# Kernel optimization log

Hardware: AMD Instinct MI355X
Metric: run time of the kernel (lower is better)

Reference implementation:

```python
import jax, jax.numpy as jnp
import numpy as np

N, E, B = 10000, 100000, 64
VOCAB, EMB, H = 5000, 100, 2000
LAYERS = 4


def setup_inputs() -> dict:
    key = jax.random.key(0)
    ks = jax.random.split(key, 12)
    s = 0.02
    tokens = jax.random.randint(ks[0], (N,), 0, VOCAB)
    edge_index = jax.random.randint(ks[1], (2, E), 0, N)
    batch = (jnp.arange(N) * B) // N  # sorted node->graph ids, every graph nonempty
    return {
        "tokens": tokens,
        "edge_index": edge_index,
        "batch": batch,
        "embed_table": jax.random.normal(ks[2], (VOCAB, EMB), jnp.float32) * s,
        "W_ggc": jax.random.normal(ks[3], (LAYERS, H, H), jnp.float32) * s,
        "W_ih": jax.random.normal(ks[4], (3 * H, H), jnp.float32) * s,
        "W_hh": jax.random.normal(ks[5], (3 * H, H), jnp.float32) * s,
        "b_ih": jnp.zeros((3 * H,), jnp.float32),
        "b_hh": jnp.zeros((3 * H,), jnp.float32),
        "conv1_w": jax.random.normal(ks[6], (50, 1, 3), jnp.float32) * s,
        "conv1_b": jnp.zeros((50,), jnp.float32),
        "conv2_w": jax.random.normal(ks[7], (100, 50, 3), jnp.float32) * s,
        "conv2_b": jnp.zeros((100,), jnp.float32),
        "conv3_w": jax.random.normal(ks[8], (150, 100, 3), jnp.float32) * s,
        "conv3_b": jnp.zeros((150,), jnp.float32),
        "lin1_w": jax.random.normal(ks[9], (500, 10950), jnp.float32) * s,
        "lin1_b": jnp.zeros((500,), jnp.float32),
        "lin2_w": jax.random.normal(ks[10], (4, 500), jnp.float32) * s,
        "lin2_b": jnp.zeros((4,), jnp.float32),
    }


def _conv1d(x, w, b):
    # x: [B, Cin, L], w: [Cout, Cin, K] -> [B, Cout, L-K+1] (VALID, like nn.Conv1d)
    y = jax.lax.conv_general_dilated(x, w, (1,), "VALID",
                                     dimension_numbers=("NCH", "OIH", "NCH"))
    return y + b[None, :, None]


def _maxpool3(x):
    # MaxPool1d(kernel=3, stride=3), floor mode (VALID)
    return jax.lax.reduce_window(x, -jnp.inf, jax.lax.max, (1, 1, 3), (1, 1, 3), "VALID")


def _gru_cell(m, h, W_ih, W_hh, b_ih, b_hh):
    gi = m @ W_ih.T + b_ih  # [N, 3H]
    gh = h @ W_hh.T + b_hh
    ir, iz, inn = jnp.split(gi, 3, axis=-1)
    hr, hz, hn = jnp.split(gh, 3, axis=-1)
    r = jax.nn.sigmoid(ir + hr)
    z = jax.nn.sigmoid(iz + hz)
    n = jnp.tanh(inn + r * hn)
    return (1.0 - z) * n + z * h


def reference(tokens, edge_index, batch, embed_table, W_ggc, W_ih, W_hh, b_ih, b_hh,
              conv1_w, conv1_b, conv2_w, conv2_b, conv3_w, conv3_b,
              lin1_w, lin1_b, lin2_w, lin2_b):
    src, dst = edge_index[0], edge_index[1]
    n_nodes = tokens.shape[0]
    # embedding + pad to GatedGraphConv width (PyG zero-pads when in < out)
    h = embed_table[tokens]                               # [N, 100]
    h = jnp.pad(h, ((0, 0), (0, H - h.shape[1])))         # [N, 2000]
    # GatedGraphConv: per-layer linear -> scatter-add over edges -> GRU update
    for i in range(LAYERS):
        m = h @ W_ggc[i]                                  # [N, H]
        agg = jax.ops.segment_sum(m[src], dst, num_segments=n_nodes)  # [N, H]
        h = _gru_cell(agg, h, W_ih, W_hh, b_ih, b_hh)
    x = jax.nn.relu(h)
    # global_max_pool over graphs
    pooled = jax.ops.segment_max(x, batch, num_segments=B)  # [B, 2000]
    x = pooled[:, None, :]                                  # [B, 1, 2000]
    x = _maxpool3(jax.nn.relu(_conv1d(x, conv1_w, conv1_b)))  # [B,50,666]
    x = _maxpool3(jax.nn.relu(_conv1d(x, conv2_w, conv2_b)))  # [B,100,221]
    x = _maxpool3(jax.nn.relu(_conv1d(x, conv3_w, conv3_b)))  # [B,150,73]
    x = x.reshape(x.shape[0], -1)                             # [B, 10950]
    x = jax.nn.relu(x @ lin1_w.T + lin1_b)
    # dropout is identity in eval mode
    x = jax.nn.relu(x @ lin2_w.T + lin2_b)
    return x
```

## Files before the change

kernel.cpp:

```cpp
#include <hip/hip_runtime.h>
#include <math.h>

#define N_NODES 10000
#define N_EDGES 100000
#define NB      64
#define EMB     100
#define H       2000
#define LAYERS  4

#define C1_OC 50
#define C1_L  666
#define C2_OC 100
#define C2_L  221
#define C3_OC 150
#define C3_L  73
#define LIN1_IN  10950
#define LIN1_OUT 500

#define SEG  2048
#define MP   10240
#define NW   2048
#define KK2  4096
#define NPACK 8192
#define NT   (KK2 / 64)

using half8 = __attribute__((ext_vector_type(8))) _Float16;
using f32x4 = __attribute__((ext_vector_type(4))) float;

__device__ inline void gload16(const void* g, void* l) {
  __builtin_amdgcn_global_load_lds(
      (const __attribute__((address_space(1))) unsigned int*)g,
      (__attribute__((address_space(3))) unsigned int*)l, 16, 0, 0);
}

__global__ void embed16_kernel(const int* __restrict__ tokens,
                               const float* __restrict__ table,
                               _Float16* __restrict__ h) {
  int n = blockIdx.x;
  int tok = tokens[n];
  for (int c = threadIdx.x; c < SEG; c += 256) {
    float v = (c < EMB) ? table[tok * EMB + c] : 0.f;
    h[(size_t)n * SEG + c] = (_Float16)v;
  }
}

__global__ void hist_kernel(const int* __restrict__ dst, int* __restrict__ counts, int e) {
  int i = blockIdx.x * 256 + threadIdx.x;
  if (i < e) atomicAdd(&counts[dst[i]], 1);
}

__global__ void scan_kernel(const int* __restrict__ counts, int* __restrict__ row_off, int n) {
  __shared__ int sums[1024];
  int tid = threadIdx.x;
  const int CH = (n + 1023) / 1024;
  int start = tid * CH;
  int local = 0;
  for (int i = 0; i < CH; i++)
    if (start + i < n) local += counts[start + i];
  sums[tid] = local;
  __syncthreads();
  for (int off = 1; off < 1024; off <<= 1) {
    int v = (tid >= off) ? sums[tid - off] : 0;
    __syncthreads();
    sums[tid] += v;
    __syncthreads();
  }
  int run = (tid > 0) ? sums[tid - 1] : 0;
  for (int i = 0; i < CH; i++)
    if (start + i < n) { row_off[start + i] = run; run += counts[start + i]; }
  if (tid == 1023) row_off[n] = run;
}

__global__ void scatter_kernel(const int* __restrict__ src, const int* __restrict__ dst,
                               const int* __restrict__ row_off, int* __restrict__ cursor,
                               int* __restrict__ csr_src, int e) {
  int i = blockIdx.x * 256 + threadIdx.x;
  if (i < e) {
    int d = dst[i];
    int pos = atomicAdd(&cursor[d], 1);
    csr_src[row_off[d] + pos] = src[i];
  }
}

__global__ void starts_kernel(const int* __restrict__ batch, int* __restrict__ starts, int n) {
  int i = blockIdx.x * 256 + threadIdx.x;
  if (i >= n) return;
  int b = batch[i];
  int pb = (i == 0) ? -1 : batch[i - 1];
  if (b != pb)
    for (int x = pb + 1; x <= b; x++) starts[x] = i;
  if (i == n - 1)
    for (int x = b + 1; x <= NB; x++) starts[x] = n;
}

__global__ void prep_wg16_kernel(const float* __restrict__ Wg, _Float16* __restrict__ out) {
  __shared__ float t[32][33];
  int l = blockIdx.z;
  const float* W = Wg + (size_t)l * H * H;
  _Float16* o = out + (size_t)l * NW * SEG;
  int kt = blockIdx.x * 32, nt = blockIdx.y * 32;
  int tx = threadIdx.x & 31, ty = threadIdx.x >> 5;
#pragma unroll
  for (int i = 0; i < 4; i++) {
    int k = kt + ty + i * 8, n = nt + tx;
    t[tx][ty + i * 8] = (k < H && n < H) ? W[(size_t)k * H + n] : 0.f;
  }
  __syncthreads();
#pragma unroll
  for (int i = 0; i < 4; i++) {
    int nl = ty + i * 8, kl = tx;
    o[(size_t)(nt + nl) * SEG + (kt + kl)] = (_Float16)t[nl][kl];
  }
}

__global__ void prep_wpack_kernel(const float* __restrict__ Wih, const float* __restrict__ Whh,
                                  _Float16* __restrict__ out) {
  int n = blockIdx.y;
  int k = blockIdx.x * 256 + threadIdx.x;
  if (k >= KK2) return;
  int gate = ((n >> 7) & 1) * 2 + ((n >> 4) & 1);
  int hcol = (n >> 8) * 64 + ((n >> 5) & 3) * 16 + (n & 15);
  float v = 0.f;
  if (hcol < H) {
    if (gate < 2) {
      int row = gate * H + hcol;
      if (k < 2048) { if (k < H) v = Wih[(size_t)row * H + k]; }
      else { int k2 = k - 2048; if (k2 < H) v = Whh[(size_t)row * H + k2]; }
    } else if (gate == 2) {
      if (k < H) v = Wih[(size_t)(2 * H + hcol) * H + k];
    } else {
      int k2 = k - 2048;
      if (k2 >= 0 && k2 < H) v = Whh[(size_t)(2 * H + hcol) * H + k2];
    }
  }
  out[(size_t)n * KK2 + k] = (_Float16)v;
}

__global__ __launch_bounds__(256) void gemm16_kernel(
    const _Float16* __restrict__ A, const _Float16* __restrict__ Bt,
    _Float16* __restrict__ C) {
  __shared__ __align__(16) _Float16 As[128][32];
  __shared__ __align__(16) _Float16 Bs[128][32];
  const int tid = threadIdx.x;
  const int wave = tid >> 6, lane = tid & 63;
  const int bm = blockIdx.y * 128, bn = blockIdx.x * 128;
  const int wm = (wave & 1) * 64, wn = (wave >> 1) * 64;
  const int srow = lane >> 2, scol = (lane & 3) * 8;
  const int fr = lane & 15, quad = lane >> 4;

  f32x4 acc[4][4];
#pragma unroll
  for (int i = 0; i < 4; i++)
#pragma unroll
    for (int j = 0; j < 4; j++) {
      f32x4 z = {0.f, 0.f, 0.f, 0.f};
      acc[i][j] = z;
    }

  for (int k0 = 0; k0 < SEG; k0 += 32) {
    gload16(A + (size_t)(bm + wave * 32 + srow) * SEG + k0 + scol, &As[wave * 32][0]);
    gload16(A + (size_t)(bm + wave * 32 + 16 + srow) * SEG + k0 + scol, &As[wave * 32 + 16][0]);
    gload16(Bt + (size_t)(bn + wave * 32 + srow) * SEG + k0 + scol, &Bs[wave * 32][0]);
    gload16(Bt + (size_t)(bn + wave * 32 + 16 + srow) * SEG + k0 + scol, &Bs[wave * 32 + 16][0]);
    __syncthreads();
    half8 af[4], bf[4];
#pragma unroll
    for (int i = 0; i < 4; i++) {
      af[i] = *(const half8*)&As[wm + i * 16 + fr][quad * 8];
      bf[i] = *(const half8*)&Bs[wn + i * 16 + fr][quad * 8];
    }
#pragma unroll
    for (int i = 0; i < 4; i++)
#pragma unroll
      for (int j = 0; j < 4; j++)
        acc[i][j] = __builtin_amdgcn_mfma_f32_16x16x32_f16(af[i], bf[j], acc[i][j], 0, 0, 0);
    __syncthreads();
  }
#pragma unroll
  for (int i = 0; i < 4; i++)
#pragma unroll
    for (int j = 0; j < 4; j++) {
      int n = bn + wn + j * 16 + fr;
      if (n >= SEG) continue;
#pragma unroll
      for (int r = 0; r < 4; r++) {
        int m = bm + wm + i * 16 + quad * 4 + r;
        C[(size_t)m * SEG + n] = (_Float16)acc[i][j][r];
      }
    }
}

__global__ void agg16_kernel(const _Float16* __restrict__ m, const int* __restrict__ row_off,
                             const int* __restrict__ csr_src, _Float16* __restrict__ agg) {
  int node = blockIdx.x;
  int s = row_off[node], e = row_off[node + 1];
  int tid = threadIdx.x;
  bool act = tid < (SEG / 8);
  float a[8] = {0, 0, 0, 0, 0, 0, 0, 0};
  __shared__ int s_src[256];
  for (int base = s; base < e; base += 256) {
    int cnt = min(256, e - base);
    __syncthreads();
    if (tid < cnt) s_src[tid] = csr_src[base + tid];
    __syncthreads();
    for (int p = 0; p < cnt; p++) {
      if (act) {
        half8 v = *(const half8*)&m[(size_t)s_src[p] * SEG + tid * 8];
#pragma unroll
        for (int i = 0; i < 8; i++) a[i] += (float)v[i];
      }
    }
  }
  if (act) {
    half8 o;
#pragma unroll
    for (int i = 0; i < 8; i++) o[i] = (_Float16)a[i];
    *(half8*)&agg[(size_t)node * SEG + tid * 8] = o;
  }
}

__global__ __launch_bounds__(512, 2) void gru2p_kernel(
    const _Float16* __restrict__ Agg, const _Float16* __restrict__ Hc,
    const _Float16* __restrict__ Wp,
    const float* __restrict__ b_ih, const float* __restrict__ b_hh,
    _Float16* __restrict__ Hn) {
  __shared__ __align__(16) _Float16 As[2][256][64];
  __shared__ __align__(16) _Float16 Bs[2][256][64];
  const int tid = threadIdx.x;
  const int wave = tid >> 6, lane = tid & 63;
  const int WM = wave >> 2, WN = wave & 3;
  const int fr = lane & 15, quad = lane >> 4;
  const int bm = blockIdx.y * 256, bn = blockIdx.x * 256;

  const int sr = lane >> 3;
  const int scl = (lane & 7) ^ sr;

  auto stageA = [&](int buf, int hf, int t) {
    const _Float16* base = (t < 32) ? Agg : Hc;
    const int k0 = (t & 31) * 64;
    const int r0 = hf * 128 + wave * 8 + sr;
#pragma unroll
    for (int c2 = 0; c2 < 2; c2++) {
      gload16(base + (size_t)(bm + r0 + c2 * 64) * SEG + k0 + scl * 8,
              &As[buf][hf * 128 + c2 * 64 + wave * 8][0]);
    }
  };
  auto stageB = [&](int buf, int hf, int t) {
    const int k0 = t * 64;
    const int r0 = hf * 128 + wave * 8 + sr;
#pragma unroll
    for (int c2 = 0; c2 < 2; c2++) {
      gload16(Wp + (size_t)(bn + r0 + c2 * 64) * KK2 + k0 + scl * 8,
              &Bs[buf][hf * 128 + c2 * 64 + wave * 8][0]);
    }
  };

  const int x0 = ((quad ^ (fr & 7)) << 3);
  const int x1 = (((quad + 4) ^ (fr & 7)) << 3);

  auto readA = [&](int buf, int mh, half8* a) {
    const _Float16* base = &As[buf][mh * 128 + WM * 64][0];
#pragma unroll
    for (int i = 0; i < 4; i++) {
      const int rb = ((i << 4) + fr) << 6;
      a[i]     = *(const half8*)&base[rb + x0];
      a[4 + i] = *(const half8*)&base[rb + x1];
    }
  };
  auto readB = [&](int buf, int nh, int j, half8* b) {
    const _Float16* base = &Bs[buf][nh * 128 + WN * 32 + (j << 4) + fr][0];
    b[0] = *(const half8*)&base[x0];
    b[1] = *(const half8*)&base[x1];
  };

  f32x4 acc[2][4][4];
#pragma unroll
  for (int a = 0; a < 2; a++)
#pragma unroll
    for (int i = 0; i < 4; i++)
#pragma unroll
      for (int g = 0; g < 4; g++) {
        f32x4 z = {0.f, 0.f, 0.f, 0.f};
        acc[a][i][g] = z;
      }

  stageA(0, 0, 0); stageA(0, 1, 0); stageB(0, 0, 0); stageB(0, 1, 0);
  stageA(1, 0, 1); stageB(1, 0, 1);
  asm volatile("s_waitcnt vmcnt(4)" ::: "memory");
  __builtin_amdgcn_s_barrier();

  half8 a0[8], a1[8], b0[2], b1[2], bx[2], bxn[2];
  readA(0, 0, a0);
  readB(0, 0, 0, b0);
  readB(0, 0, 1, b1);
  readB(0, 1, 0, bx);

  for (int t = 0; t < NT; t++) {
    const int cur = t & 1, nxt = cur ^ 1;
    const bool firstHalf = (t < 32);

    if (t + 1 < NT) { stageA(nxt, 1, t + 1); stageB(nxt, 1, t + 1); }
    asm volatile("s_waitcnt lgkmcnt(0)" ::: "memory");
    __builtin_amdgcn_sched_barrier(0);
    __builtin_amdgcn_s_barrier();
    readA(cur, 1, a1);
    __builtin_amdgcn_sched_barrier(0);
    __builtin_amdgcn_s_setprio(1);
#pragma unroll
    for (int i = 0; i < 4; i++) {
      acc[0][i][0] = __builtin_amdgcn_mfma_f32_16x16x32_f16(a0[i], b0[0], acc[0][i][0], 0, 0, 0);
      acc[0][i][1] = __builtin_amdgcn_mfma_f32_16x16x32_f16(a0[i], b1[0], acc[0][i][1], 0, 0, 0);
      acc[0][i][0] = __builtin_amdgcn_mfma_f32_16x16x32_f16(a0[4 + i], b0[1], acc[0][i][0], 0, 0, 0);
      acc[0][i][1] = __builtin_amdgcn_mfma_f32_16x16x32_f16(a0[4 + i], b1[1], acc[0][i][1], 0, 0, 0);
    }
    if (firstHalf) {
#pragma unroll
      for (int i = 0; i < 4; i++) {
        acc[0][i][2] = __builtin_amdgcn_mfma_f32_16x16x32_f16(a0[i], bx[0], acc[0][i][2], 0, 0, 0);
        acc[0][i][2] = __builtin_amdgcn_mfma_f32_16x16x32_f16(a0[4 + i], bx[1], acc[0][i][2], 0, 0, 0);
      }
    } else {
#pragma unroll
      for (int i = 0; i < 4; i++) {
        acc[0][i][3] = __builtin_amdgcn_mfma_f32_16x16x32_f16(a0[i], bx[0], acc[0][i][3], 0, 0, 0);
        acc[0][i][3] = __builtin_amdgcn_mfma_f32_16x16x32_f16(a0[4 + i], bx[1], acc[0][i][3], 0, 0, 0);
      }
    }
    __builtin_amdgcn_s_setprio(0);

    if (t + 2 < NT) {
      stageA(cur, 0, t + 2); stageB(cur, 0, t + 2);
      asm volatile("s_waitcnt vmcnt(4)" ::: "memory");
    } else {
      asm volatile("s_waitcnt vmcnt(0)" ::: "memory");
    }
    asm volatile("s_waitcnt lgkmcnt(0)" ::: "memory");
    __builtin_amdgcn_sched_barrier(0);
    __builtin_amdgcn_s_barrier();
    __builtin_amdgcn_s_setprio(1);
#pragma unroll
    for (int i = 0; i < 4; i++) {
      acc[1][i][0] = __builtin_amdgcn_mfma_f32_16x16x32_f16(a1[i], b0[0], acc[1][i][0], 0, 0, 0);
      acc[1][i][1] = __builtin_amdgcn_mfma_f32_16x16x32_f16(a1[i], b1[0], acc[1][i][1], 0, 0, 0);
      acc[1][i][0] = __builtin_amdgcn_mfma_f32_16x16x32_f16(a1[4 + i], b0[1], acc[1][i][0], 0, 0, 0);
      acc[1][i][1] = __builtin_amdgcn_mfma_f32_16x16x32_f16(a1[4 + i], b1[1], acc[1][i][1], 0, 0, 0);
    }
    __builtin_amdgcn_s_setprio(0);
    __builtin_amdgcn_sched_barrier(0);
    if (t + 1 < NT) {
      readA(nxt, 0, a0);
      readB(nxt, 0, 0, b0);
      readB(nxt, 0, 1, b1);
      readB(nxt, 1, ((t + 1) < 32) ? 0 : 1, bxn);
    }
    __builtin_amdgcn_sched_barrier(0);
    __builtin_amdgcn_s_setprio(1);
    if (firstHalf) {
#pragma unroll
      for (int i = 0; i < 4; i++) {
        acc[1][i][2] = __builtin_amdgcn_mfma_f32_16x16x32_f16(a1[i], bx[0], acc[1][i][2], 0, 0, 0);
        acc[1][i][2] = __builtin_amdgcn_mfma_f32_16x16x32_f16(a1[4 + i], bx[1], acc[1][i][2], 0, 0, 0);
      }
    } else {
#pragma unroll
      for (int i = 0; i < 4; i++) {
        acc[1][i][3] = __builtin_amdgcn_mfma_f32_16x16x32_f16(a1[i], bx[0], acc[1][i][3], 0, 0, 0);
        acc[1][i][3] = __builtin_amdgcn_mfma_f32_16x16x32_f16(a1[4 + i], bx[1], acc[1][i][3], 0, 0, 0);
      }
    }
    __builtin_amdgcn_s_setprio(0);
    bx[0] = bxn[0]; bx[1] = bxn[1];
  }

  const int c = blockIdx.x * 64 + WN * 16 + fr;
  if (c >= H) return;
  const float b_r = b_ih[c] + b_hh[c];
  const float b_z = b_ih[H + c] + b_hh[H + c];
  const float b_in = b_ih[2 * H + c];
  const float b_hn = b_hh[2 * H + c];
#pragma unroll
  for (int mh = 0; mh < 2; mh++)
#pragma unroll
    for (int i = 0; i < 4; i++)
#pragma unroll
      for (int r = 0; r < 4; r++) {
        int m = bm + mh * 128 + WM * 64 + i * 16 + quad * 4 + r;
        float rg = 1.f / (1.f + expf(-(acc[mh][i][0][r] + b_r)));
        float zg = 1.f / (1.f + expf(-(acc[mh][i][1][r] + b_z)));
        float nn = tanhf(acc[mh][i][2][r] + b_in + rg * (acc[mh][i][3][r] + b_hn));
        float hold = (float)Hc[(size_t)m * SEG + c];
        Hn[(size_t)m * SEG + c] = (_Float16)((1.f - zg) * nn + zg * hold);
      }
}

__global__ void pool16_kernel(const _Float16* __restrict__ h, const int* __restrict__ starts,
                              float* __restrict__ pooled) {
  int b = blockIdx.x;
  int s = starts[b], e = starts[b + 1];
  for (int idx = threadIdx.x; idx < H; idx += 256) {
    float mx = 0.f;
    for (int n = s; n < e; n++) mx = fmaxf(mx, (float)h[(size_t)n * SEG + idx]);
    pooled[b * H + idx] = mx;
  }
}

__global__ void conv1_kernel(const float* __restrict__ in, const float* __restrict__ w,
                             const float* __restrict__ bias, float* __restrict__ outp) {
  __shared__ float sin_[H];
  int b = blockIdx.x;
  for (int j = threadIdx.x; j < H; j += 256) sin_[j] = in[(size_t)b * H + j];
  __syncthreads();
  for (int idx = threadIdx.x; idx < C1_OC * C1_L; idx += 256) {
    int oc = idx / C1_L, t = idx % C1_L;
    float w0 = w[oc * 3], w1 = w[oc * 3 + 1], w2 = w[oc * 3 + 2];
    float bb = bias[oc];
    float best = 0.f;
    int base = t * 3;
#pragma unroll
    for (int p = 0; p < 3; p++) {
      float v = fmaf(sin_[base + p], w0, fmaf(sin_[base + p + 1], w1,
                fmaf(sin_[base + p + 2], w2, bb)));
      best = fmaxf(best, v);
    }
    outp[((size_t)b * C1_OC + oc) * C1_L + t] = best;
  }
}

__global__ void conv2_kernel(const float* __restrict__ in, const float* __restrict__ w,
                             const float* __restrict__ bias, float* __restrict__ outp) {
  int idx = blockIdx.x * 256 + threadIdx.x;
  if (idx >= NB * C2_OC * C2_L) return;
  int t = idx % C2_L;
  int rem = idx / C2_L;
  int oc = rem % C2_OC;
  int b = rem / C2_OC;
  const float* ip = in + (size_t)b * C1_OC * C1_L;
  const float* wp = w + oc * C1_OC * 3;
  float bb = bias[oc];
  float s0 = bb, s1 = bb, s2 = bb;
  int tc = t * 3;
  for (int ic = 0; ic < C1_OC; ic++) {
    const float* r = ip + ic * C1_L + tc;
    float v0 = r[0], v1 = r[1], v2 = r[2], v3 = r[3], v4 = r[4];
    float w0 = wp[ic * 3], w1 = wp[ic * 3 + 1], w2 = wp[ic * 3 + 2];
    s0 = fmaf(v0, w0, fmaf(v1, w1, fmaf(v2, w2, s0)));
    s1 = fmaf(v1, w0, fmaf(v2, w1, fmaf(v3, w2, s1)));
    s2 = fmaf(v2, w0, fmaf(v3, w1, fmaf(v4, w2, s2)));
  }
  outp[idx] = fmaxf(fmaxf(s0, fmaxf(s1, s2)), 0.f);
}

__global__ void conv3_kernel(const float* __restrict__ in, const float* __restrict__ w,
                             const float* __restrict__ bias, float* __restrict__ outp) {
  int idx = blockIdx.x * 256 + threadIdx.x;
  if (idx >= NB * C3_OC * C3_L) return;
  int t = idx % C3_L;
  int rem = idx / C3_L;
  int oc = rem % C3_OC;
  int b = rem / C3_OC;
  const float* ip = in + (size_t)b * C2_OC * C2_L;
  const float* wp = w + oc * C2_OC * 3;
  float bb = bias[oc];
  float s0 = bb, s1 = bb, s2 = bb;
  int tc = t * 3;
  for (int ic = 0; ic < C2_OC; ic++) {
    const float* r = ip + ic * C2_L + tc;
    float v0 = r[0], v1 = r[1], v2 = r[2], v3 = r[3], v4 = r[4];
    float w0 = wp[ic * 3], w1 = wp[ic * 3 + 1], w2 = wp[ic * 3 + 2];
    s0 = fmaf(v0, w0, fmaf(v1, w1, fmaf(v2, w2, s0)));
    s1 = fmaf(v1, w0, fmaf(v2, w1, fmaf(v3, w2, s1)));
    s2 = fmaf(v2, w0, fmaf(v3, w1, fmaf(v4, w2, s2)));
  }
  outp[idx] = fmaxf(fmaxf(s0, fmaxf(s1, s2)), 0.f);
}

__global__ void lin1_kernel(const float* __restrict__ x, const float* __restrict__ w,
                            const float* __restrict__ bias, float* __restrict__ outp) {
  int gid = blockIdx.x * 4 + (threadIdx.x >> 6);
  int lane = threadIdx.x & 63;
  int b = gid / LIN1_OUT;
  int o = gid % LIN1_OUT;
  const float* xp = x + (size_t)b * LIN1_IN;
  const float* wp = w + (size_t)o * LIN1_IN;
  float s = 0.f;
  for (int k = lane; k < LIN1_IN; k += 64) s = fmaf(xp[k], wp[k], s);
#pragma unroll
  for (int off = 32; off > 0; off >>= 1) s += __shfl_down(s, off, 64);
  if (lane == 0) outp[b * LIN1_OUT + o] = fmaxf(s + bias[o], 0.f);
}

__global__ void lin2_kernel(const float* __restrict__ x, const float* __restrict__ w,
                            const float* __restrict__ bias, float* __restrict__ outp) {
  int tid = threadIdx.x;
  int b = tid >> 2, o = tid & 3;
  const float* xp = x + b * LIN1_OUT;
  const float* wp = w + o * LIN1_OUT;
  float s = bias[o];
  for (int k = 0; k < LIN1_OUT; k++) s = fmaf(xp[k], wp[k], s);
  outp[b * 4 + o] = fmaxf(s, 0.f);
}

extern "C" void kernel_launch(void* const* d_in, const int* in_sizes, int n_in,
                              void* d_out, int out_size, void* d_ws, size_t ws_size,
                              hipStream_t stream) {
  const int* tokens = (const int*)d_in[0];
  const int* edge_index = (const int*)d_in[1];
  const int* batch = (const int*)d_in[2];
  const float* embed = (const float*)d_in[3];
  const float* W_ggc = (const float*)d_in[4];
  const float* W_ih = (const float*)d_in[5];
  const float* W_hh = (const float*)d_in[6];
  const float* b_ih = (const float*)d_in[7];
  const float* b_hh = (const float*)d_in[8];
  const float* c1w = (const float*)d_in[9];
  const float* c1b = (const float*)d_in[10];
  const float* c2w = (const float*)d_in[11];
  const float* c2b = (const float*)d_in[12];
  const float* c3w = (const float*)d_in[13];
  const float* c3b = (const float*)d_in[14];
  const float* l1w = (const float*)d_in[15];
  const float* l1b = (const float*)d_in[16];
  const float* l2w = (const float*)d_in[17];
  const float* l2b = (const float*)d_in[18];
  float* out = (float*)d_out;

  const int* e_src = edge_index;
  const int* e_dst = edge_index + N_EDGES;

  char* ws = (char*)d_ws;
  size_t off = 0;
  auto alloc = [&](size_t bytes) -> void* {
    void* p = ws + off;
    off = (off + bytes + 255) & ~(size_t)255;
    return p;
  };

  const size_t ACT = sizeof(_Float16) * (size_t)MP * SEG;
  _Float16* bufX = (_Float16*)alloc(ACT);
  _Float16* bufY = (_Float16*)alloc(ACT);
  _Float16* bufZ = (_Float16*)alloc(ACT);
  _Float16* Wg_b = (_Float16*)alloc(sizeof(_Float16) * (size_t)LAYERS * NW * SEG);
  _Float16* Wp   = (_Float16*)alloc(sizeof(_Float16) * (size_t)NPACK * KK2);
  int* counts = (int*)alloc(sizeof(int) * (N_NODES + 1));
  int* row_off = (int*)alloc(sizeof(int) * (N_NODES + 1));
  int* cursor = (int*)alloc(sizeof(int) * N_NODES);
  int* csr_src = (int*)alloc(sizeof(int) * N_EDGES);
  int* starts = (int*)alloc(sizeof(int) * (NB + 1));

  char* tb = (char*)bufZ;
  size_t toff = 0;
  auto talloc = [&](size_t bytes) -> void* {
    void* p = tb + toff;
    toff = (toff + bytes + 255) & ~(size_t)255;
    return p;
  };
  float* pooled = (float*)talloc(sizeof(float) * NB * H);
  float* c1 = (float*)talloc(sizeof(float) * (size_t)NB * C1_OC * C1_L);
  float* c2 = (float*)talloc(sizeof(float) * (size_t)NB * C2_OC * C2_L);
  float* c3 = (float*)talloc(sizeof(float) * (size_t)NB * C3_OC * C3_L);
  float* l1out = (float*)talloc(sizeof(float) * NB * LIN1_OUT);

  hipMemsetAsync(counts, 0, sizeof(int) * (N_NODES + 1), stream);
  hipMemsetAsync(cursor, 0, sizeof(int) * N_NODES, stream);

  {
    dim3 gg(SEG / 32, NW / 32, LAYERS);
    prep_wg16_kernel<<<gg, 256, 0, stream>>>(W_ggc, Wg_b);
    dim3 gp(KK2 / 256, NPACK);
    prep_wpack_kernel<<<gp, 256, 0, stream>>>(W_ih, W_hh, Wp);
  }

  embed16_kernel<<<N_NODES, 256, 0, stream>>>(tokens, embed, bufX);
  hist_kernel<<<(N_EDGES + 255) / 256, 256, 0, stream>>>(e_dst, counts, N_EDGES);
  scan_kernel<<<1, 1024, 0, stream>>>(counts, row_off, N_NODES);
  scatter_kernel<<<(N_EDGES + 255) / 256, 256, 0, stream>>>(e_src, e_dst, row_off, cursor,
                                                            csr_src, N_EDGES);
  starts_kernel<<<(N_NODES + 255) / 256, 256, 0, stream>>>(batch, starts, N_NODES);

  dim3 grid_m(NW / 128, MP / 128);
  dim3 grid_gru(NPACK / 256, MP / 256);
  _Float16* X = bufX;
  _Float16* Y = bufY;
  for (int l = 0; l < LAYERS; l++) {
    gemm16_kernel<<<grid_m, 256, 0, stream>>>(X, Wg_b + (size_t)l * NW * SEG, Y);
    agg16_kernel<<<N_NODES, 256, 0, stream>>>(Y, row_off, csr_src, bufZ);
    gru2p_kernel<<<grid_gru, 512, 0, stream>>>(bufZ, X, Wp, b_ih, b_hh, Y);
    _Float16* t = X; X = Y; Y = t;
  }

  pool16_kernel<<<NB, 256, 0, stream>>>(X, starts, pooled);
  conv1_kernel<<<NB, 256, 0, stream>>>(pooled, c1w, c1b, c1);
  conv2_kernel<<<(NB * C2_OC * C2_L + 255) / 256, 256, 0, stream>>>(c1, c2w, c2b, c2);
  conv3_kernel<<<(NB * C3_OC * C3_L + 255) / 256, 256, 0, stream>>>(c2, c3w, c3b, c3);
  lin1_kernel<<<NB * LIN1_OUT / 4, 256, 0, stream>>>(c3, l1w, l1b, l1out);
  lin2_kernel<<<1, 256, 0, stream>>>(l1out, l2w, l2b, out);
}
```

Baseline: 4.744 ms.

## Restructure GRU GEMM main loop to one barrier-phase with in-iteration LDS reads

Reorganises the software pipeline of the fused GRU GEMM. Each iteration now reads the current A/B fragments from LDS at its top instead of prefetching the next tile's registers at its end. The next-half and next-tile global stages are issued earlier, and MFMAs are grouped per A half (both gates plus the n-gate block together). The aim is to cut register pressure, drop the cross-iteration register handoff and one barrier-separated phase, and interleave LDS reads with MFMA issue. The cost is that LDS latency is exposed at the start of each iteration, since it is no longer hidden behind the previous MFMAs.

Result: slower. 6.785 ms (+43.0%).

```diff
diff --git a/kernel.cpp b/kernel.cpp
--- a/kernel.cpp
+++ b/kernel.cpp
@@ -219,7 +219,7 @@
   }
 }
 
-__global__ __launch_bounds__(512, 2) void gru2p_kernel(
+__global__ __launch_bounds__(512, 2) void gruv3_kernel(
     const _Float16* __restrict__ Agg, const _Float16* __restrict__ Hc,
     const _Float16* __restrict__ Wp,
     const float* __restrict__ b_ih, const float* __restrict__ b_hh,
@@ -289,87 +289,80 @@
   asm volatile("s_waitcnt vmcnt(4)" ::: "memory");
   __builtin_amdgcn_s_barrier();
 
-  half8 a0[8], a1[8], b0[2], b1[2], bx[2], bxn[2];
-  readA(0, 0, a0);
-  readB(0, 0, 0, b0);
-  readB(0, 0, 1, b1);
-  readB(0, 1, 0, bx);
-
   for (int t = 0; t < NT; t++) {
     const int cur = t & 1, nxt = cur ^ 1;
     const bool firstHalf = (t < 32);
 
+    __builtin_amdgcn_sched_barrier(0);
+    half8 a0[8], a1[8], b0[2], b1[2], bx[2];
+    readA(cur, 0, a0);
+    readB(cur, 0, 0, b0);
+    readB(cur, 0, 1, b1);
+    readB(cur, 1, firstHalf ? 0 : 1, bx);
     if (t + 1 < NT) { stageA(nxt, 1, t + 1); stageB(nxt, 1, t + 1); }
     asm volatile("s_waitcnt lgkmcnt(0)" ::: "memory");
     __builtin_amdgcn_sched_barrier(0);
     __builtin_amdgcn_s_barrier();
+    __builtin_amdgcn_sched_barrier(0);
+
     readA(cur, 1, a1);
+    if (t + 2 < NT) { stageA(cur, 0, t + 2); stageB(cur, 0, t + 2); }
+    __builtin_amdgcn_s_setprio(1);
+    if (firstHalf) {
+#pragma unroll
+      for (int i = 0; i < 4; i++) {
+        acc[0][i][0] = __builtin_amdgcn_mfma_f32_16x16x32_f16(a0[i], b0[0], acc[0][i][0], 0, 0, 0);
+        acc[0][i][1] = __builtin_amdgcn_mfma_f32_16x16x32_f16(a0[i], b1[0], acc[0][i][1], 0, 0, 0);
+        acc[0][i][2] = __builtin_amdgcn_mfma_f32_16x16x32_f16(a0[i], bx[0], acc[0][i][2], 0, 0, 0);
+        acc[0][i][0] = __builtin_amdgcn_mfma_f32_16x16x32_f16(a0[4 + i], b0[1], acc[0][i][0], 0, 0, 0);
+        acc[0][i][1] = __builtin_amdgcn_mfma_f32_16x16x32_f16(a0[4 + i], b1[1], acc[0][i][1], 0, 0, 0);
+        acc[0][i][2] = __builtin_amdgcn_mfma_f32_16x16x32_f16(a0[4 + i], bx[1], acc[0][i][2], 0, 0, 0);
+      }
+    } else {
+#pragma unroll
+      for (int i = 0; i < 4; i++) {
+        acc[0][i][0] = __builtin_amdgcn_mfma_f32_16x16x32_f16(a0[i], b0[0], acc[0][i][0], 0, 0, 0);
+        acc[0][i][1] = __builtin_amdgcn_mfma_f32_16x16x32_f16(a0[i], b1[0], acc[0][i][1], 0, 0, 0);
+        acc[0][i][3] = __builtin_amdgcn_mfma_f32_16x16x32_f16(a0[i], bx[0], acc[0][i][3], 0, 0, 0);
+        acc[0][i][0] = __builtin_amdgcn_mfma_f32_16x16x32_f16(a0[4 + i], b0[1], acc[0][i][0], 0, 0, 0);
+        acc[0][i][1] = __builtin_amdgcn_mfma_f32_16x16x32_f16(a0[4 + i], b1[1], acc[0][i][1], 0, 0, 0);
+        acc[0][i][3] = __builtin_amdgcn_mfma_f32_16x16x32_f16(a0[4 + i], bx[1], acc[0][i][3], 0, 0, 0);
+      }
+    }
+    __builtin_amdgcn_s_setprio(0);
+    asm volatile("s_waitcnt lgkmcnt(0)" ::: "memory");
     __builtin_amdgcn_sched_barrier(0);
+
     __builtin_amdgcn_s_setprio(1);
-#pragma unroll
-    for (int i = 0; i < 4; i++) {
-      acc[0][i][0] = __builtin_amdgcn_mfma_f32_16x16x32_f16(a0[i], b0[0], acc[0][i][0], 0, 0, 0);
-      acc[0][i][1] = __builtin_amdgcn_mfma_f32_16x16x32_f16(a0[i], b1[0], acc[0][i][1], 0, 0, 0);
-      acc[0][i][0] = __builtin_amdgcn_mfma_f32_16x16x32_f16(a0[4 + i], b0[1], acc[0][i][0], 0, 0, 0);
-      acc[0][i][1] = __builtin_amdgcn_mfma_f32_16x16x32_f16(a0[4 + i], b1[1], acc[0][i][1], 0, 0, 0);
-    }
     if (firstHalf) {
 #pragma unroll
       for (int i = 0; i < 4; i++) {
-        acc[0][i][2] = __builtin_amdgcn_mfma_f32_16x16x32_f16(a0[i], bx[0], acc[0][i][2], 0, 0, 0);
-        acc[0][i][2] = __builtin_amdgcn_mfma_f32_16x16x32_f16(a0[4 + i], bx[1], acc[0][i][2], 0, 0, 0);
+        acc[1][i][0] = __builtin_amdgcn_mfma_f32_16x16x32_f16(a1[i], b0[0], acc[1][i][0], 0, 0, 0);
+        acc[1][i][1] = __builtin_amdgcn_mfma_f32_16x16x32_f16(a1[i], b1[0], acc[1][i][1], 0, 0, 0);
+        acc[1][i][2] = __builtin_amdgcn_mfma_f32_16x16x32_f16(a1[i], bx[0], acc[1][i][2], 0, 0, 0);
+        acc[1][i][0] = __builtin_amdgcn_mfma_f32_16x16x32_f16(a1[4 + i], b0[1], acc[1][i][0], 0, 0, 0);
+        acc[1][i][1] = __builtin_amdgcn_mfma_f32_16x16x32_f16(a1[4 + i], b1[1], acc[1][i][1], 0, 0, 0);
+        acc[1][i][2] = __builtin_amdgcn_mfma_f32_16x16x32_f16(a1[4 + i], bx[1], acc[1][i][2], 0, 0, 0);
       }
     } else {
 #pragma unroll
       for (int i = 0; i < 4; i++) {
-        acc[0][i][3] = __builtin_amdgcn_mfma_f32_16x16x32_f16(a0[i], bx[0], acc[0][i][3], 0, 0, 0);
-        acc[0][i][3] = __builtin_amdgcn_mfma_f32_16x16x32_f16(a0[4 + i], bx[1], acc[0][i][3], 0, 0, 0);
+        acc[1][i][0] = __builtin_amdgcn_mfma_f32_16x16x32_f16(a1[i], b0[0], acc[1][i][0], 0, 0, 0);
+        acc[1][i][1] = __builtin_amdgcn_mfma_f32_16x16x32_f16(a1[i], b1[0], acc[1][i][1], 0, 0, 0);
+        acc[1][i][3] = __builtin_amdgcn_mfma_f32_16x16x32_f16(a1[i], bx[0], acc[1][i][3], 0, 0, 0);
+        acc[1][i][0] = __builtin_amdgcn_mfma_f32_16x16x32_f16(a1[4 + i], b0[1], acc[1][i][0], 0, 0, 0);
+        acc[1][i][1] = __builtin_amdgcn_mfma_f32_16x16x32_f16(a1[4 + i], b1[1], acc[1][i][1], 0, 0, 0);
+        acc[1][i][3] = __builtin_amdgcn_mfma_f32_16x16x32_f16(a1[4 + i], bx[1], acc[1][i][3], 0, 0, 0);
       }
     }
     __builtin_amdgcn_s_setprio(0);
 
     if (t + 2 < NT) {
-      stageA(cur, 0, t + 2); stageB(cur, 0, t + 2);
       asm volatile("s_waitcnt vmcnt(4)" ::: "memory");
     } else {
       asm volatile("s_waitcnt vmcnt(0)" ::: "memory");
     }
-    asm volatile("s_waitcnt lgkmcnt(0)" ::: "memory");
-    __builtin_amdgcn_sched_barrier(0);
     __builtin_amdgcn_s_barrier();
-    __builtin_amdgcn_s_setprio(1);
-#pragma unroll
-    for (int i = 0; i < 4; i++) {
-      acc[1][i][0] = __builtin_amdgcn_mfma_f32_16x16x32_f16(a1[i], b0[0], acc[1][i][0], 0, 0, 0);
-      acc[1][i][1] = __builtin_amdgcn_mfma_f32_16x16x32_f16(a1[i], b1[0], acc[1][i][1], 0, 0, 0);
-      acc[1][i][0] = __builtin_amdgcn_mfma_f32_16x16x32_f16(a1[4 + i], b0[1], acc[1][i][0], 0, 0, 0);
-      acc[1][i][1] = __builtin_amdgcn_mfma_f32_16x16x32_f16(a1[4 + i], b1[1], acc[1][i][1], 0, 0, 0);
-    }
-    __builtin_amdgcn_s_setprio(0);
-    __builtin_amdgcn_sched_barrier(0);
-    if (t + 1 < NT) {
-      readA(nxt, 0, a0);
-      readB(nxt, 0, 0, b0);
-      readB(nxt, 0, 1, b1);
-      readB(nxt, 1, ((t + 1) < 32) ? 0 : 1, bxn);
-    }
-    __builtin_amdgcn_sched_barrier(0);
-    __builtin_amdgcn_s_setprio(1);
-    if (firstHalf) {
-#pragma unroll
-      for (int i = 0; i < 4; i++) {
-        acc[1][i][2] = __builtin_amdgcn_mfma_f32_16x16x32_f16(a1[i], bx[0], acc[1][i][2], 0, 0, 0);
-        acc[1][i][2] = __builtin_amdgcn_mfma_f32_16x16x32_f16(a1[4 + i], bx[1], acc[1][i][2], 0, 0, 0);
-      }
-    } else {
-#pragma unroll
-      for (int i = 0; i < 4; i++) {
-        acc[1][i][3] = __builtin_amdgcn_mfma_f32_16x16x32_f16(a1[i], bx[0], acc[1][i][3], 0, 0, 0);
-        acc[1][i][3] = __builtin_amdgcn_mfma_f32_16x16x32_f16(a1[4 + i], bx[1], acc[1][i][3], 0, 0, 0);
-      }
-    }
-    __builtin_amdgcn_s_setprio(0);
-    bx[0] = bxn[0]; bx[1] = bxn[1];
   }
 
   const int c = blockIdx.x * 64 + WN * 16 + fr;
@@ -584,7 +577,7 @@
   for (int l = 0; l < LAYERS; l++) {
     gemm16_kernel<<<grid_m, 256, 0, stream>>>(X, Wg_b + (size_t)l * NW * SEG, Y);
     agg16_kernel<<<N_NODES, 256, 0, stream>>>(Y, row_off, csr_src, bufZ);
-    gru2p_kernel<<<grid_gru, 512, 0, stream>>>(bufZ, X, Wp, b_ih, b_hh, Y);
+    gruv3_kernel<<<grid_gru, 512, 0, stream>>>(bufZ, X, Wp, b_ih, b_hh, Y);
     _Float16* t = X; X = Y; Y = t;
   }
 
```
